# Kernel optimization log

Hardware: AMD Instinct MI355X
Metric: run time of the kernel (lower is better)

## Reference

```python
import jax, jax.numpy as jnp
import numpy as np

MARGIN = 0.2
EPS = 1e-6


def setup_inputs() -> dict:
    key = jax.random.key(0)
    k1, k2 = jax.random.split(key)
    B, C = 8192, 1024
    z_label = jax.random.randint(k1, (B,), 0, 256, dtype=jnp.int64 if jax.config.jax_enable_x64 else jnp.int32)
    z_idx = jnp.arange(B, dtype=z_label.dtype)
    z = jax.random.normal(k2, (B, C), dtype=jnp.float32)
    return {"z_label": z_label, "z_idx": z_idx, "z": z}


def reference(z_label, z_idx, z):
    B = z.shape[0]
    k = max(2, int(B * 0.01))  # static: labels overwritten if batch has a single unique label
    all_same = jnp.all(z_label == z_label[0])
    z_label = jnp.where(all_same & (jnp.arange(B) < k), -1, z_label)

    # Vectorized triplet mining (replaces per-sample Python loop):
    # positive: first j with same label, different sample idx; negative: first j with different label.
    label_eq = z_label[:, None] == z_label[None, :]            # [B, B]
    pos_mask = label_eq & (z_idx[:, None] != z_idx[None, :])   # [B, B]
    neg_mask = ~label_eq                                       # [B, B]
    pos_idx = jnp.argmax(pos_mask, axis=1)  # first True (torch.where(...)[0][0])
    neg_idx = jnp.argmax(neg_mask, axis=1)
    valid = pos_mask.any(axis=1) & neg_mask.any(axis=1)        # [B]

    # TripletMarginLoss (p=2, swap=False): d(x,y) = ||x - y + eps||_2
    a, p_emb, n_emb = z, z[pos_idx], z[neg_idx]
    d_ap = jnp.sqrt(jnp.sum((a - p_emb + EPS) ** 2, axis=1))
    d_an = jnp.sqrt(jnp.sum((a - n_emb + EPS) ** 2, axis=1))
    per = jnp.maximum(d_ap - d_an + MARGIN, 0.0)               # [B]

    n_valid = valid.sum()
    vf = valid.astype(per.dtype)
    loss = jnp.where(n_valid > 0,
                     jnp.sum(per * vf) / jnp.maximum(n_valid, 1).astype(per.dtype),
                     jnp.array(0.0, per.dtype))
    return loss
```

## Files before the change

### kernel.cpp

```cpp
#include <hip/hip_runtime.h>

#define MARGIN 0.2f
#define EPSC 1e-6f

__device__ inline void acc8(const float4& av, const float4& pv, const float4& nv,
                            float& sap, float& san) {
    float d;
    d = av.x - pv.x + EPSC; sap += d * d;
    d = av.y - pv.y + EPSC; sap += d * d;
    d = av.z - pv.z + EPSC; sap += d * d;
    d = av.w - pv.w + EPSC; sap += d * d;
    d = av.x - nv.x + EPSC; san += d * d;
    d = av.y - nv.y + EPSC; san += d * d;
    d = av.z - nv.z + EPSC; san += d * d;
    d = av.w - nv.w + EPSC; san += d * d;
}

__device__ inline void scan4(const int4& lj, const int4& xj, int li, int myidx,
                             int j0, int& pos, int& neg) {
    if (pos < 0) {
        int m = ((lj.x == li && xj.x != myidx) ? 1 : 0)
              | ((lj.y == li && xj.y != myidx) ? 2 : 0)
              | ((lj.z == li && xj.z != myidx) ? 4 : 0)
              | ((lj.w == li && xj.w != myidx) ? 8 : 0);
        unsigned long long b = __ballot(m != 0);
        if (b) {
            int L  = __ffsll(b) - 1;
            int mL = __shfl(m, L, 64);
            pos = j0 + L * 4 + (__ffs(mL) - 1);
        }
    }
    if (neg < 0) {
        int m = ((lj.x != li) ? 1 : 0) | ((lj.y != li) ? 2 : 0)
              | ((lj.z != li) ? 4 : 0) | ((lj.w != li) ? 8 : 0);
        unsigned long long b = __ballot(m != 0);
        if (b) {
            int L  = __ffsll(b) - 1;
            int mL = __shfl(m, L, 64);
            neg = j0 + L * 4 + (__ffs(mL) - 1);
        }
    }
}

__device__ inline void mine_row_64(const int* __restrict__ label,
                                   const int* __restrict__ zidx, int B, int lane,
                                   int li, int myidx, int& pos, int& neg) {
    pos = -1; neg = -1;
    for (int j0 = 0; j0 < B && (pos < 0 || neg < 0); j0 += 64) {
        int j = j0 + lane;
        bool inb = j < B;
        int lj = 0, xj = 0;
        if (inb) { lj = label[j]; xj = zidx[j]; }
        unsigned long long pb = __ballot(inb && lj == li && xj != myidx);
        unsigned long long nb = __ballot(inb && lj != li);
        if (pos < 0 && pb) pos = j0 + __ffsll(pb) - 1;
        if (neg < 0 && nb) neg = j0 + __ffsll(nb) - 1;
    }
}

__device__ inline void mine_allsame(const int* __restrict__ zidx, int B, int lane,
                                    int i, int myidx, int& pos, int& neg) {
    int k = B / 100; if (k < 2) k = 2;
    int kk = k < B ? k : B;
    int lo, hi;
    if (i < kk) { lo = 0;  hi = kk; neg = (kk < B) ? kk : -1; }
    else        { lo = kk; hi = B;  neg = 0; }
    pos = -1;
    for (int j0 = lo; j0 < hi && pos < 0; j0 += 64) {
        int j = j0 + lane;
        bool ok = (j < hi) && (zidx[j] != myidx);
        unsigned long long b = __ballot(ok);
        if (b) pos = j0 + __ffsll(b) - 1;
    }
}

__global__ __launch_bounds__(256) void dist_kernel(
    const float* __restrict__ z, const int* __restrict__ label,
    const int* __restrict__ zidx, int B, int C, float2* __restrict__ g_part)
{
    const int wave = threadIdx.x >> 6;
    const int lane = threadIdx.x & 63;
    const int ia = blockIdx.x * 8 + wave * 2;
    const int ib = ia + 1;
    const bool hasA = ia < B, hasB = ib < B;
    const bool c1024 = (C == 1024);

    float lsum = 0.f, lcnt = 0.f;

    int liA = 0, idxA = 0, liB = 0, idxB = 0;
    if (hasA) { liA = label[ia]; idxA = zidx[ia]; }
    if (hasB) { liB = label[ib]; idxB = zidx[ib]; }

    const float4* aA = (const float4*)(z + (size_t)ia * C) + lane;
    const float4* aB = (const float4*)(z + (size_t)ib * C) + lane;
    float4 A0, A1, A2, A3, Bb0, Bb1, Bb2, Bb3;
    if (hasA && c1024) { A0 = aA[0]; A1 = aA[64]; A2 = aA[128]; A3 = aA[192]; }
    if (hasB && c1024) { Bb0 = aB[0]; Bb1 = aB[64]; Bb2 = aB[128]; Bb3 = aB[192]; }

    int posA = -1, negA = -1, posB = -1, negB = -1;
    if (hasA) {
        if ((B & 255) == 0) {
            if (!hasB) { posB = 0; negB = 0; }
            for (int j0 = 0; j0 < B && (posA < 0 || negA < 0 || posB < 0 || negB < 0);
                 j0 += 256) {
                const int base = j0 + lane * 4;
                int4 lj = *(const int4*)(label + base);
                int4 xj = *(const int4*)(zidx + base);
                scan4(lj, xj, liA, idxA, j0, posA, negA);
                if (hasB) scan4(lj, xj, liB, idxB, j0, posB, negB);
            }
        } else {
            mine_row_64(label, zidx, B, lane, liA, idxA, posA, negA);
            if (hasB) mine_row_64(label, zidx, B, lane, liB, idxB, posB, negB);
        }
        if (negA < 0) {
            mine_allsame(zidx, B, lane, ia, idxA, posA, negA);
            if (hasB) mine_allsame(zidx, B, lane, ib, idxB, posB, negB);
        }
    }

    if (hasA) {
        const int pi = posA < 0 ? 0 : posA;
        const int ni = negA < 0 ? 0 : negA;
        const float4* p = (const float4*)(z + (size_t)pi * C) + lane;
        const float4* n = (const float4*)(z + (size_t)ni * C) + lane;
        float sap = 0.f, san = 0.f;
        if (c1024) {
            float4 p0 = p[0], p1 = p[64], p2 = p[128], p3 = p[192];
            float4 n0 = n[0], n1 = n[64], n2 = n[128], n3 = n[192];
            acc8(A0, p0, n0, sap, san); acc8(A1, p1, n1, sap, san);
            acc8(A2, p2, n2, sap, san); acc8(A3, p3, n3, sap, san);
        } else {
            const float4* a = (const float4*)(z + (size_t)ia * C) + lane;
            const int nk = C >> 8;
            for (int kk = 0; kk < nk; ++kk)
                acc8(a[kk * 64], p[kk * 64], n[kk * 64], sap, san);
            for (int c = (nk << 8) + lane; c < C; c += 64) {
                float av = z[(size_t)ia * C + c];
                float pv = z[(size_t)pi * C + c];
                float nv = z[(size_t)ni * C + c];
                float d = av - pv + EPSC; sap += d * d;
                d = av - nv + EPSC; san += d * d;
            }
        }
        for (int off = 32; off; off >>= 1) {
            sap += __shfl_xor(sap, off, 64);
            san += __shfl_xor(san, off, 64);
        }
        if (lane == 0 && posA >= 0 && negA >= 0) {
            lsum += fmaxf(sqrtf(sap) - sqrtf(san) + MARGIN, 0.f);
            lcnt += 1.f;
        }
    }

    if (hasB) {
        const int pi = posB < 0 ? 0 : posB;
        const int ni = negB < 0 ? 0 : negB;
        const float4* p = (const float4*)(z + (size_t)pi * C) + lane;
        const float4* n = (const float4*)(z + (size_t)ni * C) + lane;
        float sap = 0.f, san = 0.f;
        if (c1024) {
            float4 p0 = p[0], p1 = p[64], p2 = p[128], p3 = p[192];
            float4 n0 = n[0], n1 = n[64], n2 = n[128], n3 = n[192];
            acc8(Bb0, p0, n0, sap, san); acc8(Bb1, p1, n1, sap, san);
            acc8(Bb2, p2, n2, sap, san); acc8(Bb3, p3, n3, sap, san);
        } else {
            const float4* a = (const float4*)(z + (size_t)ib * C) + lane;
            const int nk = C >> 8;
            for (int kk = 0; kk < nk; ++kk)
                acc8(a[kk * 64], p[kk * 64], n[kk * 64], sap, san);
            for (int c = (nk << 8) + lane; c < C; c += 64) {
                float av = z[(size_t)ib * C + c];
                float pv = z[(size_t)pi * C + c];
                float nv = z[(size_t)ni * C + c];
                float d = av - pv + EPSC; sap += d * d;
                d = av - nv + EPSC; san += d * d;
            }
        }
        for (int off = 32; off; off >>= 1) {
            sap += __shfl_xor(sap, off, 64);
            san += __shfl_xor(san, off, 64);
        }
        if (lane == 0 && posB >= 0 && negB >= 0) {
            lsum += fmaxf(sqrtf(sap) - sqrtf(san) + MARGIN, 0.f);
            lcnt += 1.f;
        }
    }

    __shared__ float s_sum[4], s_cnt[4];
    if (lane == 0) { s_sum[wave] = lsum; s_cnt[wave] = lcnt; }
    __syncthreads();
    if (threadIdx.x == 0) {
        float bs = 0.f, bc = 0.f;
        for (int w = 0; w < 4; ++w) { bs += s_sum[w]; bc += s_cnt[w]; }
        g_part[blockIdx.x] = make_float2(bs, bc);
    }
}

__global__ __launch_bounds__(1024) void final_kernel(
    const float2* __restrict__ g_part, int nb, float* __restrict__ out)
{
    const int t = threadIdx.x;
    float s = 0.f, c = 0.f;
    for (int idx = t; idx < nb; idx += blockDim.x) {
        float2 v = g_part[idx];
        s += v.x; c += v.y;
    }
    for (int off = 32; off; off >>= 1) {
        s += __shfl_xor(s, off, 64);
        c += __shfl_xor(c, off, 64);
    }
    __shared__ float s_s[16], s_c[16];
    const int wave = t >> 6, lane = t & 63;
    if (lane == 0) { s_s[wave] = s; s_c[wave] = c; }
    __syncthreads();
    if (t == 0) {
        float ts = 0.f, tc = 0.f;
        const int nw = blockDim.x >> 6;
        for (int w = 0; w < nw; ++w) { ts += s_s[w]; tc += s_c[w]; }
        out[0] = (tc > 0.f) ? ts / tc : 0.f;
    }
}

extern "C" void kernel_launch(void* const* d_in, const int* in_sizes, int n_in,
                              void* d_out, int out_size, void* d_ws, size_t ws_size,
                              hipStream_t stream) {
    const int*   z_label = (const int*)d_in[0];
    const int*   z_idx   = (const int*)d_in[1];
    const float* z       = (const float*)d_in[2];
    const int B = in_sizes[0];
    const int C = in_sizes[2] / B;
    float* out = (float*)d_out;

    const int nblk = (B + 7) / 8;
    float2* g_part = (float2*)d_ws;

    dist_kernel<<<nblk, 256, 0, stream>>>(z, z_label, z_idx, B, C, g_part);
    final_kernel<<<1, 1024, 0, stream>>>(g_part, nblk, out);
}
```

Before: 84.92 us.

## Split triplet mining into a separate kernel writing pos/neg indices

Moves the positive/negative index search out of the distance kernel into its own kernel, with one wave per row, and stores the pos/neg pairs in workspace. The distance kernel then loads the precomputed indices and reads the anchor row afterwards instead of prefetching it. This gives more parallelism in the mining scan and simplifies the distance kernel. In exchange it adds a kernel launch and a global round-trip for the indices, and the mining scans no longer share label loads between two rows.

After: 85.17 us. About the same (+0.3%).

```diff
diff --git a/kernel.cpp b/kernel.cpp
--- a/kernel.cpp
+++ b/kernel.cpp
@@ -74,9 +74,38 @@
     }
 }
 
+__global__ __launch_bounds__(256) void mine_kernel(
+    const int* __restrict__ label, const int* __restrict__ zidx,
+    int B, int2* __restrict__ pn)
+{
+    const int wave = threadIdx.x >> 6;
+    const int lane = threadIdx.x & 63;
+    const int i = blockIdx.x * 4 + wave;
+    if (i >= B) return;
+
+    const int li = label[i];
+    const int myidx = zidx[i];
+    int pos = -1, neg = -1;
+
+    if ((B & 255) == 0) {
+        for (int j0 = 0; j0 < B && (pos < 0 || neg < 0); j0 += 256) {
+            const int base = j0 + lane * 4;
+            int4 lj = *(const int4*)(label + base);
+            int4 xj = *(const int4*)(zidx + base);
+            scan4(lj, xj, li, myidx, j0, pos, neg);
+        }
+    } else {
+        mine_row_64(label, zidx, B, lane, li, myidx, pos, neg);
+    }
+    if (neg < 0)
+        mine_allsame(zidx, B, lane, i, myidx, pos, neg);
+
+    if (lane == 0) pn[i] = make_int2(pos, neg);
+}
+
 __global__ __launch_bounds__(256) void dist_kernel(
-    const float* __restrict__ z, const int* __restrict__ label,
-    const int* __restrict__ zidx, int B, int C, float2* __restrict__ g_part)
+    const float* __restrict__ z, const int2* __restrict__ pn,
+    int B, int C, float2* __restrict__ g_part)
 {
     const int wave = threadIdx.x >> 6;
     const int lane = threadIdx.x & 63;
@@ -87,51 +116,23 @@
 
     float lsum = 0.f, lcnt = 0.f;
 
-    int liA = 0, idxA = 0, liB = 0, idxB = 0;
-    if (hasA) { liA = label[ia]; idxA = zidx[ia]; }
-    if (hasB) { liB = label[ib]; idxB = zidx[ib]; }
-
-    const float4* aA = (const float4*)(z + (size_t)ia * C) + lane;
-    const float4* aB = (const float4*)(z + (size_t)ib * C) + lane;
-    float4 A0, A1, A2, A3, Bb0, Bb1, Bb2, Bb3;
-    if (hasA && c1024) { A0 = aA[0]; A1 = aA[64]; A2 = aA[128]; A3 = aA[192]; }
-    if (hasB && c1024) { Bb0 = aB[0]; Bb1 = aB[64]; Bb2 = aB[128]; Bb3 = aB[192]; }
-
-    int posA = -1, negA = -1, posB = -1, negB = -1;
+    int2 pnA = hasA ? pn[ia] : make_int2(0, 0);
+    int2 pnB = hasB ? pn[ib] : make_int2(0, 0);
+
     if (hasA) {
-        if ((B & 255) == 0) {
-            if (!hasB) { posB = 0; negB = 0; }
-            for (int j0 = 0; j0 < B && (posA < 0 || negA < 0 || posB < 0 || negB < 0);
-                 j0 += 256) {
-                const int base = j0 + lane * 4;
-                int4 lj = *(const int4*)(label + base);
-                int4 xj = *(const int4*)(zidx + base);
-                scan4(lj, xj, liA, idxA, j0, posA, negA);
-                if (hasB) scan4(lj, xj, liB, idxB, j0, posB, negB);
-            }
-        } else {
-            mine_row_64(label, zidx, B, lane, liA, idxA, posA, negA);
-            if (hasB) mine_row_64(label, zidx, B, lane, liB, idxB, posB, negB);
-        }
-        if (negA < 0) {
-            mine_allsame(zidx, B, lane, ia, idxA, posA, negA);
-            if (hasB) mine_allsame(zidx, B, lane, ib, idxB, posB, negB);
-        }
-    }
-
-    if (hasA) {
-        const int pi = posA < 0 ? 0 : posA;
-        const int ni = negA < 0 ? 0 : negA;
+        const int pi = pnA.x < 0 ? 0 : pnA.x;
+        const int ni = pnA.y < 0 ? 0 : pnA.y;
+        const float4* a = (const float4*)(z + (size_t)ia * C) + lane;
         const float4* p = (const float4*)(z + (size_t)pi * C) + lane;
         const float4* n = (const float4*)(z + (size_t)ni * C) + lane;
         float sap = 0.f, san = 0.f;
         if (c1024) {
+            float4 A0 = a[0], A1 = a[64], A2 = a[128], A3 = a[192];
             float4 p0 = p[0], p1 = p[64], p2 = p[128], p3 = p[192];
             float4 n0 = n[0], n1 = n[64], n2 = n[128], n3 = n[192];
             acc8(A0, p0, n0, sap, san); acc8(A1, p1, n1, sap, san);
             acc8(A2, p2, n2, sap, san); acc8(A3, p3, n3, sap, san);
         } else {
-            const float4* a = (const float4*)(z + (size_t)ia * C) + lane;
             const int nk = C >> 8;
             for (int kk = 0; kk < nk; ++kk)
                 acc8(a[kk * 64], p[kk * 64], n[kk * 64], sap, san);
@@ -147,25 +148,26 @@
             sap += __shfl_xor(sap, off, 64);
             san += __shfl_xor(san, off, 64);
         }
-        if (lane == 0 && posA >= 0 && negA >= 0) {
+        if (lane == 0 && pnA.x >= 0 && pnA.y >= 0) {
             lsum += fmaxf(sqrtf(sap) - sqrtf(san) + MARGIN, 0.f);
             lcnt += 1.f;
         }
     }
 
     if (hasB) {
-        const int pi = posB < 0 ? 0 : posB;
-        const int ni = negB < 0 ? 0 : negB;
+        const int pi = pnB.x < 0 ? 0 : pnB.x;
+        const int ni = pnB.y < 0 ? 0 : pnB.y;
+        const float4* a = (const float4*)(z + (size_t)ib * C) + lane;
         const float4* p = (const float4*)(z + (size_t)pi * C) + lane;
         const float4* n = (const float4*)(z + (size_t)ni * C) + lane;
         float sap = 0.f, san = 0.f;
         if (c1024) {
+            float4 A0 = a[0], A1 = a[64], A2 = a[128], A3 = a[192];
             float4 p0 = p[0], p1 = p[64], p2 = p[128], p3 = p[192];
             float4 n0 = n[0], n1 = n[64], n2 = n[128], n3 = n[192];
-            acc8(Bb0, p0, n0, sap, san); acc8(Bb1, p1, n1, sap, san);
-            acc8(Bb2, p2, n2, sap, san); acc8(Bb3, p3, n3, sap, san);
+            acc8(A0, p0, n0, sap, san); acc8(A1, p1, n1, sap, san);
+            acc8(A2, p2, n2, sap, san); acc8(A3, p3, n3, sap, san);
         } else {
-            const float4* a = (const float4*)(z + (size_t)ib * C) + lane;
             const int nk = C >> 8;
             for (int kk = 0; kk < nk; ++kk)
                 acc8(a[kk * 64], p[kk * 64], n[kk * 64], sap, san);
@@ -181,7 +183,7 @@
             sap += __shfl_xor(sap, off, 64);
             san += __shfl_xor(san, off, 64);
         }
-        if (lane == 0 && posB >= 0 && negB >= 0) {
+        if (lane == 0 && pnB.x >= 0 && pnB.y >= 0) {
             lsum += fmaxf(sqrtf(sap) - sqrtf(san) + MARGIN, 0.f);
             lcnt += 1.f;
         }
@@ -234,7 +236,10 @@
 
     const int nblk = (B + 7) / 8;
     float2* g_part = (float2*)d_ws;
-
-    dist_kernel<<<nblk, 256, 0, stream>>>(z, z_label, z_idx, B, C, g_part);
+    size_t pn_off = ((size_t)nblk * sizeof(float2) + 255) & ~(size_t)255;
+    int2* pn = (int2*)((char*)d_ws + pn_off);
+
+    mine_kernel<<<(B + 3) / 4, 256, 0, stream>>>(z_label, z_idx, B, pn);
+    dist_kernel<<<nblk, 256, 0, stream>>>(z, pn, B, C, g_part);
     final_kernel<<<1, 1024, 0, stream>>>(g_part, nblk, out);
 }
```
